# Kernel optimization log

Measured on AMD Instinct MI355X. Metric: run time of the kernel, lower is better.

Reference implementation:

```python
import jax, jax.numpy as jnp
import numpy as np

B, T, C = 2, 1024, 1024
E, F, K = 8, 2048, 2


def setup_inputs() -> dict:
    key = jax.random.key(0)
    ks = jax.random.split(key, 5)
    s = 1.0 / np.sqrt(C)
    return {
        "x": jax.random.normal(ks[0], (B, T, C), jnp.float32),
        "Wr": jax.random.normal(ks[1], (E, C), jnp.float32) * s,   # router weight [E, d_model]
        "w1": jax.random.normal(ks[2], (E, C, F), jnp.float32) * s, # gate proj per expert
        "w3": jax.random.normal(ks[3], (E, C, F), jnp.float32) * s, # up proj per expert
        "w2": jax.random.normal(ks[4], (E, F, C), jnp.float32) * (1.0 / np.sqrt(F)),  # down proj
    }


def reference(x, Wr, w1, w3, w2):
    Bq, Tq, Cq = x.shape
    flat = x.reshape(-1, Cq)                          # [N, C]
    N = flat.shape[0]
    probs = jax.nn.softmax(flat @ Wr.T, axis=-1)      # [N, E]
    topw, topi = jax.lax.top_k(probs, K)              # [N, K]
    topw = topw / jnp.sum(topw, axis=-1, keepdims=True)
    # dense gate matrix: zero for unselected experts (same math as masked loop)
    gates = jnp.zeros((N, E), flat.dtype).at[jnp.arange(N)[:, None], topi].set(topw)
    # evaluate all experts, weight by gates (gate=0 kills unrouted experts)
    h1 = jnp.einsum('nd,edf->nef', flat, w1)          # [N, E, F]
    h3 = jnp.einsum('nd,edf->nef', flat, w3)
    h = jax.nn.silu(h1) * h3
    y = jnp.einsum('nef,efd->ned', h, w2)             # [N, E, C]
    out = jnp.einsum('ned,ne->nd', y, gates)          # [N, C]
    return out.reshape(Bq, Tq, Cq)
```

## Files before the change

kernel.cpp:

```cpp
#include <hip/hip_runtime.h>
#include <math.h>

typedef _Float16 f16;
typedef _Float16 f16x2 __attribute__((ext_vector_type(2)));
typedef _Float16 f16x4 __attribute__((ext_vector_type(4)));
typedef _Float16 f16x8 __attribute__((ext_vector_type(8)));
typedef __fp16 h16x2 __attribute__((ext_vector_type(2)));
typedef float f32x4 __attribute__((ext_vector_type(4)));
typedef float f32x16 __attribute__((ext_vector_type(16)));

#define N_TOK 2048
#define C_DIM 1024
#define E_NUM 8
#define F_DIM 2048
#define BM 256

#define WS_COUNTS    0
#define WS_OFFSETS   64
#define WS_CURSOR    192
#define WS_TOPI      256
#define WS_TOPW      (WS_TOPI + 16384)
#define WS_ROWS      (WS_TOPW + 16384)
#define WS_SLOT      (WS_ROWS + 16384)
#define WS_X16       (1u << 20)
#define WS_H         (6u << 20)
#define WS_Y0        (23u << 20)
#define WS_Y1        (32u << 20)

__device__ __forceinline__ void glds16(const void* g, void* l) {
  __builtin_amdgcn_global_load_lds((const __attribute__((address_space(1))) void*)g,
                                   (__attribute__((address_space(3))) void*)l, 16, 0, 0);
}

__device__ __forceinline__ f16x2 pkrtz(float a, float b) {
  union { h16x2 h; f16x2 f; } u;
  u.h = __builtin_amdgcn_cvt_pkrtz(a, b);
  return u.f;
}

__global__ void cvtx_kernel(const float* __restrict__ x, f16* __restrict__ x16) {
  int i = (blockIdx.x * 256 + threadIdx.x) * 8;
  f32x4 a = *(const f32x4*)(x + i);
  f32x4 b = *(const f32x4*)(x + i + 4);
  union { f16x8 v; f16x2 h[4]; } u;
  u.h[0] = pkrtz(a[0], a[1]);
  u.h[1] = pkrtz(a[2], a[3]);
  u.h[2] = pkrtz(b[0], b[1]);
  u.h[3] = pkrtz(b[2], b[3]);
  *(f16x8*)(x16 + i) = u.v;
}

__global__ void router_kernel(const float* __restrict__ x, const float* __restrict__ Wr,
                              int* counts, int* topi, float* topw) {
  int tok = blockIdx.x * 4 + (threadIdx.x >> 6);
  int lane = threadIdx.x & 63;
  const float* xr = x + (size_t)tok * C_DIM;
  float xv[16];
#pragma unroll
  for (int i = 0; i < 16; ++i) xv[i] = xr[i * 64 + lane];
  float logit[E_NUM];
#pragma unroll
  for (int e = 0; e < E_NUM; ++e) {
    const float* wr = Wr + (size_t)e * C_DIM;
    float acc = 0.f;
#pragma unroll
    for (int i = 0; i < 16; ++i) acc += xv[i] * wr[i * 64 + lane];
#pragma unroll
    for (int s = 1; s < 64; s <<= 1) acc += __shfl_xor(acc, s, 64);
    logit[e] = acc;
  }
  if (lane == 0) {
    float m = logit[0];
#pragma unroll
    for (int e = 1; e < E_NUM; ++e) m = fmaxf(m, logit[e]);
    float p[E_NUM];
#pragma unroll
    for (int e = 0; e < E_NUM; ++e) p[e] = expf(logit[e] - m);
    float p0 = -1.f, p1 = -1.f;
    int i0 = 0, i1 = 0;
#pragma unroll
    for (int e = 0; e < E_NUM; ++e) {
      float v = p[e];
      if (v > p0) { p1 = p0; i1 = i0; p0 = v; i0 = e; }
      else if (v > p1) { p1 = v; i1 = e; }
    }
    float inv = 1.f / (p0 + p1);
    topi[2 * tok] = i0; topi[2 * tok + 1] = i1;
    topw[2 * tok] = p0 * inv; topw[2 * tok + 1] = p1 * inv;
    atomicAdd(&counts[i0], 1);
    atomicAdd(&counts[i1], 1);
  }
}

__global__ void scan_kernel(const int* counts, int* offsets, int* cursor) {
  if (threadIdx.x == 0) {
    int o = 0;
    for (int e = 0; e < E_NUM; ++e) {
      offsets[e] = o; cursor[e] = o;
      o += counts[e];
    }
    offsets[E_NUM] = o;
  }
}

__global__ void scatter_kernel(const int* __restrict__ topi, int* cursor,
                               int* rows_perm, int* slot_of) {
  int n = blockIdx.x * blockDim.x + threadIdx.x;
  if (n >= N_TOK) return;
#pragma unroll
  for (int k = 0; k < 2; ++k) {
    int e = topi[2 * n + k];
    int pos = atomicAdd(&cursor[e], 1);
    rows_perm[pos] = n;
    slot_of[2 * n + k] = pos;
  }
}

#define UP_STEP(R1, R3)                                                          \
  do {                                                                           \
    { union { f16x8 v; f16x2 h[4]; } u;                                          \
      u.h[0] = pkrtz(R1[0], R1[1]); u.h[1] = pkrtz(R1[2], R1[3]);                \
      u.h[2] = pkrtz(R1[4], R1[5]); u.h[3] = pkrtz(R1[6], R1[7]);                \
      *(f16x8*)&B1_lds[cur][bso] = u.v;                                          \
      u.h[0] = pkrtz(R3[0], R3[1]); u.h[1] = pkrtz(R3[2], R3[3]);                \
      u.h[2] = pkrtz(R3[4], R3[5]); u.h[3] = pkrtz(R3[6], R3[7]);                \
      *(f16x8*)&B3_lds[cur][bso] = u.v; }                                        \
    asm volatile("s_waitcnt lgkmcnt(0)" ::: "memory");                           \
    __builtin_amdgcn_s_barrier();                                                \
    { int kn = ((ti + 2) & 31) * 32;                                             \
      _Pragma("unroll") for (int j = 0; j < 8; ++j) {                            \
        R1[j] = w1p[(size_t)(kn + j) * F_DIM];                                   \
        R3[j] = w3p[(size_t)(kn + j) * F_DIM]; }                                 \
      glds16(asrc[0] + kn, a_wr + wid * 512);                                    \
      glds16(asrc[1] + kn, a_wr + (8 + wid) * 512); }                            \
    asm volatile("s_waitcnt vmcnt(36)" ::: "memory");                            \
    { f16x8 a[2][2], b[2][2];                                                    \
      _Pragma("unroll") for (int mi = 0; mi < 2; ++mi)                           \
        _Pragma("unroll") for (int kk = 0; kk < 2; ++kk) {                       \
          int row = wr + mi * 32 + ln31;                                         \
          int cell = kk * 2 + fh;                                                \
          a[mi][kk] = *(const f16x8*)&a_rd0[row * 32 + (cell ^ ((row >> 1) & 3)) * 8]; } \
      _Pragma("unroll") for (int ni = 0; ni < 2; ++ni)                           \
        _Pragma("unroll") for (int kk = 0; kk < 2; ++kk) {                       \
          int col = wc + ni * 32 + ln31;                                         \
          int cell = kk * 2 + fh;                                                \
          b[ni][kk] = *(const f16x8*)&B1_lds[cur][col * 32 + (cell ^ ((col >> 1) & 3)) * 8]; } \
      _Pragma("unroll") for (int kk = 0; kk < 2; ++kk)                           \
        _Pragma("unroll") for (int mi = 0; mi < 2; ++mi)                         \
          _Pragma("unroll") for (int ni = 0; ni < 2; ++ni)                       \
            acc1[mi][ni] = __builtin_amdgcn_mfma_f32_32x32x16_f16(a[mi][kk], b[ni][kk], acc1[mi][ni], 0, 0, 0); \
      _Pragma("unroll") for (int ni = 0; ni < 2; ++ni)                           \
        _Pragma("unroll") for (int kk = 0; kk < 2; ++kk) {                       \
          int col = wc + ni * 32 + ln31;                                         \
          int cell = kk * 2 + fh;                                                \
          b[ni][kk] = *(const f16x8*)&B3_lds[cur][col * 32 + (cell ^ ((col >> 1) & 3)) * 8]; } \
      _Pragma("unroll") for (int kk = 0; kk < 2; ++kk)                           \
        _Pragma("unroll") for (int mi = 0; mi < 2; ++mi)                         \
          _Pragma("unroll") for (int ni = 0; ni < 2; ++ni)                       \
            acc3[mi][ni] = __builtin_amdgcn_mfma_f32_32x32x16_f16(a[mi][kk], b[ni][kk], acc3[mi][ni], 0, 0, 0); } \
    { f16* _t = a_rd0; a_rd0 = a_rd1; a_rd1 = a_wr; a_wr = _t; }                 \
    ++ti; cur ^= 1;                                                              \
  } while (0)

__launch_bounds__(512, 2)
__global__ void upproj_kernel(const f16* __restrict__ x16,
                              const float* __restrict__ w1,
                              const float* __restrict__ w3,
                              const int* __restrict__ counts,
                              const int* __restrict__ offsets,
                              const int* __restrict__ rows_perm,
                              f16* __restrict__ h_buf) {
  __shared__ f16 A_lds[3][BM * 32];
  __shared__ f16 B1_lds[2][128 * 32];
  __shared__ f16 B3_lds[2][128 * 32];

  int bid = blockIdx.x;
  int e = bid & 7;
  int slot = bid >> 3;
  int tile = slot & 7;
  int fidx = slot >> 3;
  int cnt = counts[e];
  if (tile * BM >= cnt) return;
  int row0 = tile * BM;
  int off = offsets[e];
  int f0 = fidx * 128;
  int t = threadIdx.x, wid = t >> 6, lane = t & 63;
  int ln31 = lane & 31, fh = lane >> 5;

  const f16* asrc[2];
#pragma unroll
  for (int p = 0; p < 2; ++p) {
    int c = (p * 8 + wid) * 64 + lane;
    int row = c >> 2, cc = c & 3;
    int lr = row0 + row; if (lr > cnt - 1) lr = cnt - 1;
    int g = rows_perm[off + lr];
    asrc[p] = x16 + (size_t)g * C_DIM + 8 * (cc ^ ((row >> 1) & 3));
  }

  int bcol = t & 127, kg = t >> 7;
  int bso = bcol * 32 + (kg ^ ((bcol >> 1) & 3)) * 8;
  const size_t eb = (size_t)e * C_DIM * F_DIM;
  const float* w1p = w1 + eb + (size_t)(kg * 8) * F_DIM + f0 + bcol;
  const float* w3p = w3 + eb + (size_t)(kg * 8) * F_DIM + f0 + bcol;

  f32x16 acc1[2][2] = {};
  f32x16 acc3[2][2] = {};
  int wr = (wid >> 1) * 64, wc = (wid & 1) * 64;

  f16* a_rd0 = &A_lds[0][0];
  f16* a_rd1 = &A_lds[1][0];
  f16* a_wr  = &A_lds[2][0];

  float rA1[8], rA3[8], rB1[8], rB3[8];
#pragma unroll
  for (int j = 0; j < 8; ++j) { rA1[j] = w1p[(size_t)j * F_DIM]; rA3[j] = w3p[(size_t)j * F_DIM]; }
  glds16(asrc[0], a_rd0 + wid * 512);
  glds16(asrc[1], a_rd0 + (8 + wid) * 512);
#pragma unroll
  for (int j = 0; j < 8; ++j) { rB1[j] = w1p[(size_t)(32 + j) * F_DIM]; rB3[j] = w3p[(size_t)(32 + j) * F_DIM]; }
  glds16(asrc[0] + 32, a_rd1 + wid * 512);
  glds16(asrc[1] + 32, a_rd1 + (8 + wid) * 512);

  int ti = 0, cur = 0;
  for (int tp = 0; tp < 16; ++tp) {
    UP_STEP(rA1, rA3);
    UP_STEP(rB1, rB3);
  }

#pragma unroll
  for (int mi = 0; mi < 2; ++mi)
#pragma unroll
    for (int ni = 0; ni < 2; ++ni)
#pragma unroll
      for (int i = 0; i < 16; ++i) {
        int rr = (i & 3) + 8 * (i >> 2) + 4 * fh;
        int lr = row0 + wr + mi * 32 + rr;
        if (lr < cnt) {
          float v1 = acc1[mi][ni][i], v3 = acc3[mi][ni][i];
          float hval = v1 / (1.f + expf(-v1)) * v3;
          h_buf[(size_t)(off + lr) * F_DIM + f0 + wc + ni * 32 + ln31] = (f16)hval;
        }
      }
}

#define DN_STEP(RB)                                                              \
  do {                                                                           \
    { union { f16x8 v; f16x2 h[4]; } u;                                          \
      u.h[0] = pkrtz(RB[0], RB[1]); u.h[1] = pkrtz(RB[2], RB[3]);                \
      u.h[2] = pkrtz(RB[4], RB[5]); u.h[3] = pkrtz(RB[6], RB[7]);                \
      *(f16x8*)&B_lds[cur][bso] = u.v; }                                         \
    asm volatile("s_waitcnt lgkmcnt(0)" ::: "memory");                           \
    __builtin_amdgcn_s_barrier();                                                \
    { int kn = ((ti + 2) & 31) * 32;                                             \
      _Pragma("unroll") for (int j = 0; j < 8; ++j)                              \
        RB[j] = w2p[(size_t)(kn + j) * C_DIM];                                   \
      glds16(asrc[0] + kn, a_wr + wid * 512);                                    \
      glds16(asrc[1] + kn, a_wr + (8 + wid) * 512); }                            \
    asm volatile("s_waitcnt vmcnt(20)" ::: "memory");                            \
    { f16x8 a[2][2], b[2][2];                                                    \
      _Pragma("unroll") for (int mi = 0; mi < 2; ++mi)                           \
        _Pragma("unroll") for (int kk = 0; kk < 2; ++kk) {                       \
          int row = wr + mi * 32 + ln31;                                         \
          int cell = kk * 2 + fh;                                                \
          a[mi][kk] = *(const f16x8*)&a_rd0[row * 32 + (cell ^ ((row >> 1) & 3)) * 8]; } \
      _Pragma("unroll") for (int ni = 0; ni < 2; ++ni)                           \
        _Pragma("unroll") for (int kk = 0; kk < 2; ++kk) {                       \
          int col = wc + ni * 32 + ln31;                                         \
          int cell = kk * 2 + fh;                                                \
          b[ni][kk] = *(const f16x8*)&B_lds[cur][col * 32 + (cell ^ ((col >> 1) & 3)) * 8]; } \
      _Pragma("unroll") for (int kk = 0; kk < 2; ++kk)                           \
        _Pragma("unroll") for (int mi = 0; mi < 2; ++mi)                         \
          _Pragma("unroll") for (int ni = 0; ni < 2; ++ni)                       \
            acc[mi][ni] = __builtin_amdgcn_mfma_f32_32x32x16_f16(a[mi][kk], b[ni][kk], acc[mi][ni], 0, 0, 0); } \
    { f16* _t = a_rd0; a_rd0 = a_rd1; a_rd1 = a_wr; a_wr = _t; }                 \
    ++ti; cur ^= 1;                                                              \
  } while (0)

__launch_bounds__(512, 2)
__global__ void downproj_kernel(const f16* __restrict__ h_buf,
                                const float* __restrict__ w2,
                                const int* __restrict__ counts,
                                const int* __restrict__ offsets,
                                f16* __restrict__ y0,
                                f16* __restrict__ y1) {
  __shared__ f16 A_lds[3][BM * 32];
  __shared__ f16 B_lds[2][128 * 32];

  int bid = blockIdx.x;
  int e = bid & 7;
  int slot = bid >> 3;
  int tile = slot & 7;
  int kh = (slot >> 3) & 1;
  int cidx = slot >> 4;
  int cnt = counts[e];
  if (tile * BM >= cnt) return;
  f16* yb = kh ? y1 : y0;
  int row0 = tile * BM;
  int off = offsets[e];
  int c0 = cidx * 128;
  int t = threadIdx.x, wid = t >> 6, lane = t & 63;
  int ln31 = lane & 31, fh = lane >> 5;

  const f16* asrc[2];
#pragma unroll
  for (int p = 0; p < 2; ++p) {
    int c = (p * 8 + wid) * 64 + lane;
    int row = c >> 2, cc = c & 3;
    int lr = row0 + row; if (lr > cnt - 1) lr = cnt - 1;
    asrc[p] = h_buf + (size_t)(off + lr) * F_DIM + kh * 1024 + 8 * (cc ^ ((row >> 1) & 3));
  }

  int bcol = t & 127, kg = t >> 7;
  int bso = bcol * 32 + (kg ^ ((bcol >> 1) & 3)) * 8;
  const float* w2p = w2 + (size_t)e * F_DIM * C_DIM
                     + (size_t)(kh * 1024 + kg * 8) * C_DIM + c0 + bcol;

  f32x16 acc[2][2] = {};
  int wr = (wid >> 1) * 64, wc = (wid & 1) * 64;

  f16* a_rd0 = &A_lds[0][0];
  f16* a_rd1 = &A_lds[1][0];
  f16* a_wr  = &A_lds[2][0];

  float rA[8], rB[8];
#pragma unroll
  for (int j = 0; j < 8; ++j) rA[j] = w2p[(size_t)j * C_DIM];
  glds16(asrc[0], a_rd0 + wid * 512);
  glds16(asrc[1], a_rd0 + (8 + wid) * 512);
#pragma unroll
  for (int j = 0; j < 8; ++j) rB[j] = w2p[(size_t)(32 + j) * C_DIM];
  glds16(asrc[0] + 32, a_rd1 + wid * 512);
  glds16(asrc[1] + 32, a_rd1 + (8 + wid) * 512);

  int ti = 0, cur = 0;
  for (int tp = 0; tp < 16; ++tp) {
    DN_STEP(rA);
    DN_STEP(rB);
  }

#pragma unroll
  for (int mi = 0; mi < 2; ++mi)
#pragma unroll
    for (int ni = 0; ni < 2; ++ni)
#pragma unroll
      for (int i = 0; i < 16; ++i) {
        int rr = (i & 3) + 8 * (i >> 2) + 4 * fh;
        int lr = row0 + wr + mi * 32 + rr;
        if (lr < cnt)
          yb[(size_t)(off + lr) * C_DIM + c0 + wc + ni * 32 + ln31] = (f16)acc[mi][ni][i];
      }
}

__global__ void combine_kernel(const f16* __restrict__ y0, const f16* __restrict__ y1,
                               const int* __restrict__ slot_of,
                               const float* __restrict__ topw,
                               float* __restrict__ out) {
  int n = blockIdx.x;
  int s0 = slot_of[2 * n], s1 = slot_of[2 * n + 1];
  float g0 = topw[2 * n], g1 = topw[2 * n + 1];
  int c = threadIdx.x * 4;
  f16x4 a0 = *(const f16x4*)(y0 + (size_t)s0 * C_DIM + c);
  f16x4 a1 = *(const f16x4*)(y1 + (size_t)s0 * C_DIM + c);
  f16x4 b0 = *(const f16x4*)(y0 + (size_t)s1 * C_DIM + c);
  f16x4 b1 = *(const f16x4*)(y1 + (size_t)s1 * C_DIM + c);
  f32x4 o;
#pragma unroll
  for (int i = 0; i < 4; ++i)
    o[i] = g0 * ((float)a0[i] + (float)a1[i]) + g1 * ((float)b0[i] + (float)b1[i]);
  *(f32x4*)(out + (size_t)n * C_DIM + c) = o;
}

extern "C" void kernel_launch(void* const* d_in, const int* in_sizes, int n_in,
                              void* d_out, int out_size, void* d_ws, size_t ws_size,
                              hipStream_t stream) {
  const float* x  = (const float*)d_in[0];
  const float* Wr = (const float*)d_in[1];
  const float* w1 = (const float*)d_in[2];
  const float* w3 = (const float*)d_in[3];
  const float* w2 = (const float*)d_in[4];
  float* out = (float*)d_out;
  char* ws = (char*)d_ws;

  int* counts    = (int*)(ws + WS_COUNTS);
  int* offsets   = (int*)(ws + WS_OFFSETS);
  int* cursor    = (int*)(ws + WS_CURSOR);
  int* topi      = (int*)(ws + WS_TOPI);
  float* topw    = (float*)(ws + WS_TOPW);
  int* rows_perm = (int*)(ws + WS_ROWS);
  int* slot_of   = (int*)(ws + WS_SLOT);
  f16* x16       = (f16*)(ws + WS_X16);
  f16* h_buf     = (f16*)(ws + WS_H);
  f16* y0        = (f16*)(ws + WS_Y0);
  f16* y1        = (f16*)(ws + WS_Y1);

  (void)hipMemsetAsync(ws, 0, 256, stream);
  cvtx_kernel<<<N_TOK * C_DIM / 8 / 256, 256, 0, stream>>>(x, x16);
  router_kernel<<<N_TOK / 4, 256, 0, stream>>>(x, Wr, counts, topi, topw);
  scan_kernel<<<1, 64, 0, stream>>>(counts, offsets, cursor);
  scatter_kernel<<<N_TOK / 256, 256, 0, stream>>>(topi, cursor, rows_perm, slot_of);
  upproj_kernel<<<E_NUM * 128, 512, 0, stream>>>(
      x16, w1, w3, counts, offsets, rows_perm, h_buf);
  downproj_kernel<<<E_NUM * 128, 512, 0, stream>>>(
      h_buf, w2, counts, offsets, y0, y1);
  combine_kernel<<<N_TOK, 256, 0, stream>>>(y0, y1, slot_of, topw, out);
}
```

Before: 240.1 us.

## Pre-transpose weights to fp16 and stream all GEMM operands directly into LDS

Adds a per-call kernel that converts w1, w3 and w2 to fp16 and transposes them to a K-contiguous layout. The up- and down-projection GEMMs can then load the weight tiles with direct global-to-LDS loads into a triple-buffered pipeline, instead of loading fp32 into registers, converting, and storing to LDS. It also reorders block indexing so that neighbouring blocks share weight columns, and raises MFMA issue priority. The cost is an extra full read and write pass over all expert weights on every call.

```diff
diff --git a/kernel.cpp b/kernel.cpp
--- a/kernel.cpp
+++ b/kernel.cpp
@@ -22,10 +22,13 @@
 #define WS_TOPW      (WS_TOPI + 16384)
 #define WS_ROWS      (WS_TOPW + 16384)
 #define WS_SLOT      (WS_ROWS + 16384)
-#define WS_X16       (1u << 20)
-#define WS_H         (6u << 20)
-#define WS_Y0        (23u << 20)
-#define WS_Y1        (32u << 20)
+#define WS_X16       (1ull << 20)
+#define WS_H         (6ull << 20)
+#define WS_Y0        (23ull << 20)
+#define WS_Y1        (32ull << 20)
+#define WS_W1T       (48ull << 20)
+#define WS_W3T       (80ull << 20)
+#define WS_W2T       (112ull << 20)
 
 __device__ __forceinline__ void glds16(const void* g, void* l) {
   __builtin_amdgcn_global_load_lds((const __attribute__((address_space(1))) void*)g,
@@ -50,6 +53,41 @@
   *(f16x8*)(x16 + i) = u.v;
 }
 
+__global__ void wt_kernel(const float* __restrict__ w1, const float* __restrict__ w3,
+                          const float* __restrict__ w2,
+                          f16* __restrict__ w1t, f16* __restrict__ w3t, f16* __restrict__ w2t) {
+  __shared__ __align__(16) f16 T[128 * 132];
+  int tid = blockIdx.x;
+  int m = tid >> 10;
+  int r = tid & 1023;
+  int e = r >> 7;
+  int tl = r & 127;
+  const float* src; f16* dst; int K, Fd, kt, ft;
+  if (m == 2) { K = F_DIM; Fd = C_DIM; kt = tl >> 3; ft = tl & 7; src = w2; dst = w2t; }
+  else        { K = C_DIM; Fd = F_DIM; kt = tl >> 4; ft = tl & 15; src = (m ? w3 : w1); dst = (m ? w3t : w1t); }
+  src += ((size_t)e * K + kt * 128) * Fd + ft * 128;
+  dst += ((size_t)e * Fd + ft * 128) * K + kt * 128;
+  int t = threadIdx.x;
+  int rr = t >> 5, c4 = (t & 31) * 4;
+#pragma unroll
+  for (int it = 0; it < 16; ++it) {
+    int k = it * 8 + rr;
+    f32x4 v = *(const f32x4*)(src + (size_t)k * Fd + c4);
+    union { f16x4 q; f16x2 h[2]; } u;
+    u.h[0] = pkrtz(v[0], v[1]); u.h[1] = pkrtz(v[2], v[3]);
+    *(f16x4*)&T[k * 132 + c4] = u.q;
+  }
+  __syncthreads();
+  int f = t >> 1, kh = t & 1;
+#pragma unroll
+  for (int j8 = 0; j8 < 8; ++j8) {
+    union { f16x8 v; f16 s[8]; } u;
+#pragma unroll
+    for (int jj = 0; jj < 8; ++jj) u.s[jj] = T[(kh * 64 + j8 * 8 + jj) * 132 + f];
+    *(f16x8*)(dst + (size_t)f * K + kh * 64 + j8 * 8) = u.v;
+  }
+}
+
 __global__ void router_kernel(const float* __restrict__ x, const float* __restrict__ Wr,
                               int* counts, int* topi, float* topw) {
   int tok = blockIdx.x * 4 + (threadIdx.x >> 6);
@@ -116,69 +154,57 @@
   }
 }
 
-#define UP_STEP(R1, R3)                                                          \
+#define ROT3(P0, P1, P2) { f16* _t = P0; P0 = P1; P1 = P2; P2 = _t; }
+
+#define UP_MFMA()                                                                \
   do {                                                                           \
-    { union { f16x8 v; f16x2 h[4]; } u;                                          \
-      u.h[0] = pkrtz(R1[0], R1[1]); u.h[1] = pkrtz(R1[2], R1[3]);                \
-      u.h[2] = pkrtz(R1[4], R1[5]); u.h[3] = pkrtz(R1[6], R1[7]);                \
-      *(f16x8*)&B1_lds[cur][bso] = u.v;                                          \
-      u.h[0] = pkrtz(R3[0], R3[1]); u.h[1] = pkrtz(R3[2], R3[3]);                \
-      u.h[2] = pkrtz(R3[4], R3[5]); u.h[3] = pkrtz(R3[6], R3[7]);                \
-      *(f16x8*)&B3_lds[cur][bso] = u.v; }                                        \
-    asm volatile("s_waitcnt lgkmcnt(0)" ::: "memory");                           \
-    __builtin_amdgcn_s_barrier();                                                \
-    { int kn = ((ti + 2) & 31) * 32;                                             \
-      _Pragma("unroll") for (int j = 0; j < 8; ++j) {                            \
-        R1[j] = w1p[(size_t)(kn + j) * F_DIM];                                   \
-        R3[j] = w3p[(size_t)(kn + j) * F_DIM]; }                                 \
-      glds16(asrc[0] + kn, a_wr + wid * 512);                                    \
-      glds16(asrc[1] + kn, a_wr + (8 + wid) * 512); }                            \
-    asm volatile("s_waitcnt vmcnt(36)" ::: "memory");                            \
-    { f16x8 a[2][2], b[2][2];                                                    \
+    f16x8 a[2][2], b[2][2];                                                      \
+    _Pragma("unroll") for (int mi = 0; mi < 2; ++mi)                             \
+      _Pragma("unroll") for (int kk = 0; kk < 2; ++kk) {                         \
+        int row = wr + mi * 32 + ln31;                                           \
+        int cell = kk * 2 + fh;                                                  \
+        a[mi][kk] = *(const f16x8*)&a_c[row * 32 + (cell ^ ((row >> 1) & 3)) * 8]; } \
+    _Pragma("unroll") for (int ni = 0; ni < 2; ++ni)                             \
+      _Pragma("unroll") for (int kk = 0; kk < 2; ++kk) {                         \
+        int col = wc + ni * 32 + ln31;                                           \
+        int cell = kk * 2 + fh;                                                  \
+        b[ni][kk] = *(const f16x8*)&b1_c[col * 32 + (cell ^ ((col >> 1) & 3)) * 8]; } \
+    __builtin_amdgcn_s_setprio(1);                                               \
+    _Pragma("unroll") for (int kk = 0; kk < 2; ++kk)                             \
       _Pragma("unroll") for (int mi = 0; mi < 2; ++mi)                           \
-        _Pragma("unroll") for (int kk = 0; kk < 2; ++kk) {                       \
-          int row = wr + mi * 32 + ln31;                                         \
-          int cell = kk * 2 + fh;                                                \
-          a[mi][kk] = *(const f16x8*)&a_rd0[row * 32 + (cell ^ ((row >> 1) & 3)) * 8]; } \
-      _Pragma("unroll") for (int ni = 0; ni < 2; ++ni)                           \
-        _Pragma("unroll") for (int kk = 0; kk < 2; ++kk) {                       \
-          int col = wc + ni * 32 + ln31;                                         \
-          int cell = kk * 2 + fh;                                                \
-          b[ni][kk] = *(const f16x8*)&B1_lds[cur][col * 32 + (cell ^ ((col >> 1) & 3)) * 8]; } \
-      _Pragma("unroll") for (int kk = 0; kk < 2; ++kk)                           \
-        _Pragma("unroll") for (int mi = 0; mi < 2; ++mi)                         \
-          _Pragma("unroll") for (int ni = 0; ni < 2; ++ni)                       \
-            acc1[mi][ni] = __builtin_amdgcn_mfma_f32_32x32x16_f16(a[mi][kk], b[ni][kk], acc1[mi][ni], 0, 0, 0); \
-      _Pragma("unroll") for (int ni = 0; ni < 2; ++ni)                           \
-        _Pragma("unroll") for (int kk = 0; kk < 2; ++kk) {                       \
-          int col = wc + ni * 32 + ln31;                                         \
-          int cell = kk * 2 + fh;                                                \
-          b[ni][kk] = *(const f16x8*)&B3_lds[cur][col * 32 + (cell ^ ((col >> 1) & 3)) * 8]; } \
-      _Pragma("unroll") for (int kk = 0; kk < 2; ++kk)                           \
-        _Pragma("unroll") for (int mi = 0; mi < 2; ++mi)                         \
-          _Pragma("unroll") for (int ni = 0; ni < 2; ++ni)                       \
-            acc3[mi][ni] = __builtin_amdgcn_mfma_f32_32x32x16_f16(a[mi][kk], b[ni][kk], acc3[mi][ni], 0, 0, 0); } \
-    { f16* _t = a_rd0; a_rd0 = a_rd1; a_rd1 = a_wr; a_wr = _t; }                 \
-    ++ti; cur ^= 1;                                                              \
+        _Pragma("unroll") for (int ni = 0; ni < 2; ++ni)                         \
+          acc1[mi][ni] = __builtin_amdgcn_mfma_f32_32x32x16_f16(a[mi][kk], b[ni][kk], acc1[mi][ni], 0, 0, 0); \
+    __builtin_amdgcn_s_setprio(0);                                               \
+    _Pragma("unroll") for (int ni = 0; ni < 2; ++ni)                             \
+      _Pragma("unroll") for (int kk = 0; kk < 2; ++kk) {                         \
+        int col = wc + ni * 32 + ln31;                                           \
+        int cell = kk * 2 + fh;                                                  \
+        b[ni][kk] = *(const f16x8*)&b3_c[col * 32 + (cell ^ ((col >> 1) & 3)) * 8]; } \
+    __builtin_amdgcn_s_setprio(1);                                               \
+    _Pragma("unroll") for (int kk = 0; kk < 2; ++kk)                             \
+      _Pragma("unroll") for (int mi = 0; mi < 2; ++mi)                           \
+        _Pragma("unroll") for (int ni = 0; ni < 2; ++ni)                         \
+          acc3[mi][ni] = __builtin_amdgcn_mfma_f32_32x32x16_f16(a[mi][kk], b[ni][kk], acc3[mi][ni], 0, 0, 0); \
+    __builtin_amdgcn_s_setprio(0);                                               \
   } while (0)
 
 __launch_bounds__(512, 2)
 __global__ void upproj_kernel(const f16* __restrict__ x16,
-                              const float* __restrict__ w1,
-                              const float* __restrict__ w3,
+                              const f16* __restrict__ w1t,
+                              const f16* __restrict__ w3t,
                               const int* __restrict__ counts,
                               const int* __restrict__ offsets,
                               const int* __restrict__ rows_perm,
                               f16* __restrict__ h_buf) {
-  __shared__ f16 A_lds[3][BM * 32];
-  __shared__ f16 B1_lds[2][128 * 32];
-  __shared__ f16 B3_lds[2][128 * 32];
+  __shared__ __align__(16) f16 A_lds[3][BM * 32];
+  __shared__ __align__(16) f16 B1_lds[3][128 * 32];
+  __shared__ __align__(16) f16 B3_lds[3][128 * 32];
 
   int bid = blockIdx.x;
   int e = bid & 7;
   int slot = bid >> 3;
-  int tile = slot & 7;
-  int fidx = slot >> 3;
+  int fidx = slot & 15;
+  int tile = slot >> 4;
   int cnt = counts[e];
   if (tile * BM >= cnt) return;
   int row0 = tile * BM;
@@ -190,42 +216,55 @@
   const f16* asrc[2];
 #pragma unroll
   for (int p = 0; p < 2; ++p) {
-    int c = (p * 8 + wid) * 64 + lane;
+    int c = p * 512 + t;
     int row = c >> 2, cc = c & 3;
     int lr = row0 + row; if (lr > cnt - 1) lr = cnt - 1;
     int g = rows_perm[off + lr];
     asrc[p] = x16 + (size_t)g * C_DIM + 8 * (cc ^ ((row >> 1) & 3));
   }
-
-  int bcol = t & 127, kg = t >> 7;
-  int bso = bcol * 32 + (kg ^ ((bcol >> 1) & 3)) * 8;
-  const size_t eb = (size_t)e * C_DIM * F_DIM;
-  const float* w1p = w1 + eb + (size_t)(kg * 8) * F_DIM + f0 + bcol;
-  const float* w3p = w3 + eb + (size_t)(kg * 8) * F_DIM + f0 + bcol;
+  int bcol = t >> 2, bcc = t & 3;
+  int bswz = 8 * (bcc ^ ((bcol >> 1) & 3));
+  const f16* b1src = w1t + (size_t)e * F_DIM * C_DIM + (size_t)(f0 + bcol) * C_DIM + bswz;
+  const f16* b3src = w3t + (size_t)e * F_DIM * C_DIM + (size_t)(f0 + bcol) * C_DIM + bswz;
 
   f32x16 acc1[2][2] = {};
   f32x16 acc3[2][2] = {};
   int wr = (wid >> 1) * 64, wc = (wid & 1) * 64;
 
-  f16* a_rd0 = &A_lds[0][0];
-  f16* a_rd1 = &A_lds[1][0];
-  f16* a_wr  = &A_lds[2][0];
-
-  float rA1[8], rA3[8], rB1[8], rB3[8];
-#pragma unroll
-  for (int j = 0; j < 8; ++j) { rA1[j] = w1p[(size_t)j * F_DIM]; rA3[j] = w3p[(size_t)j * F_DIM]; }
-  glds16(asrc[0], a_rd0 + wid * 512);
-  glds16(asrc[1], a_rd0 + (8 + wid) * 512);
-#pragma unroll
-  for (int j = 0; j < 8; ++j) { rB1[j] = w1p[(size_t)(32 + j) * F_DIM]; rB3[j] = w3p[(size_t)(32 + j) * F_DIM]; }
-  glds16(asrc[0] + 32, a_rd1 + wid * 512);
-  glds16(asrc[1] + 32, a_rd1 + (8 + wid) * 512);
-
-  int ti = 0, cur = 0;
-  for (int tp = 0; tp < 16; ++tp) {
-    UP_STEP(rA1, rA3);
-    UP_STEP(rB1, rB3);
-  }
+  f16 *a_c = &A_lds[0][0], *a_n = &A_lds[1][0], *a_f = &A_lds[2][0];
+  f16 *b1_c = &B1_lds[0][0], *b1_n = &B1_lds[1][0], *b1_f = &B1_lds[2][0];
+  f16 *b3_c = &B3_lds[0][0], *b3_n = &B3_lds[1][0], *b3_f = &B3_lds[2][0];
+
+  glds16(asrc[0], a_c + wid * 512);
+  glds16(asrc[1], a_c + (8 + wid) * 512);
+  glds16(b1src, b1_c + wid * 512);
+  glds16(b3src, b3_c + wid * 512);
+  glds16(asrc[0] + 32, a_n + wid * 512);
+  glds16(asrc[1] + 32, a_n + (8 + wid) * 512);
+  glds16(b1src + 32, b1_n + wid * 512);
+  glds16(b3src + 32, b3_n + wid * 512);
+
+  for (int tt = 0; tt < 30; ++tt) {
+    asm volatile("s_waitcnt vmcnt(4)" ::: "memory");
+    __builtin_amdgcn_s_barrier();
+    asm volatile("" ::: "memory");
+    int kn = (tt + 2) * 32;
+    glds16(asrc[0] + kn, a_f + wid * 512);
+    glds16(asrc[1] + kn, a_f + (8 + wid) * 512);
+    glds16(b1src + kn, b1_f + wid * 512);
+    glds16(b3src + kn, b3_f + wid * 512);
+    UP_MFMA();
+    ROT3(a_c, a_n, a_f); ROT3(b1_c, b1_n, b1_f); ROT3(b3_c, b3_n, b3_f);
+  }
+  asm volatile("s_waitcnt vmcnt(4)" ::: "memory");
+  __builtin_amdgcn_s_barrier();
+  asm volatile("" ::: "memory");
+  UP_MFMA();
+  ROT3(a_c, a_n, a_f); ROT3(b1_c, b1_n, b1_f); ROT3(b3_c, b3_n, b3_f);
+  asm volatile("s_waitcnt vmcnt(0)" ::: "memory");
+  __builtin_amdgcn_s_barrier();
+  asm volatile("" ::: "memory");
+  UP_MFMA();
 
 #pragma unroll
   for (int mi = 0; mi < 2; ++mi)
@@ -243,55 +282,43 @@
       }
 }
 
-#define DN_STEP(RB)                                                              \
+#define DN_MFMA()                                                                \
   do {                                                                           \
-    { union { f16x8 v; f16x2 h[4]; } u;                                          \
-      u.h[0] = pkrtz(RB[0], RB[1]); u.h[1] = pkrtz(RB[2], RB[3]);                \
-      u.h[2] = pkrtz(RB[4], RB[5]); u.h[3] = pkrtz(RB[6], RB[7]);                \
-      *(f16x8*)&B_lds[cur][bso] = u.v; }                                         \
-    asm volatile("s_waitcnt lgkmcnt(0)" ::: "memory");                           \
-    __builtin_amdgcn_s_barrier();                                                \
-    { int kn = ((ti + 2) & 31) * 32;                                             \
-      _Pragma("unroll") for (int j = 0; j < 8; ++j)                              \
-        RB[j] = w2p[(size_t)(kn + j) * C_DIM];                                   \
-      glds16(asrc[0] + kn, a_wr + wid * 512);                                    \
-      glds16(asrc[1] + kn, a_wr + (8 + wid) * 512); }                            \
-    asm volatile("s_waitcnt vmcnt(20)" ::: "memory");                            \
-    { f16x8 a[2][2], b[2][2];                                                    \
+    f16x8 a[2][2], b[2][2];                                                      \
+    _Pragma("unroll") for (int mi = 0; mi < 2; ++mi)                             \
+      _Pragma("unroll") for (int kk = 0; kk < 2; ++kk) {                         \
+        int row = wr + mi * 32 + ln31;                                           \
+        int cell = kk * 2 + fh;                                                  \
+        a[mi][kk] = *(const f16x8*)&a_c[row * 32 + (cell ^ ((row >> 1) & 3)) * 8]; } \
+    _Pragma("unroll") for (int ni = 0; ni < 2; ++ni)                             \
+      _Pragma("unroll") for (int kk = 0; kk < 2; ++kk) {                         \
+        int col = wc + ni * 32 + ln31;                                           \
+        int cell = kk * 2 + fh;                                                  \
+        b[ni][kk] = *(const f16x8*)&b_c[col * 32 + (cell ^ ((col >> 1) & 3)) * 8]; } \
+    __builtin_amdgcn_s_setprio(1);                                               \
+    _Pragma("unroll") for (int kk = 0; kk < 2; ++kk)                             \
       _Pragma("unroll") for (int mi = 0; mi < 2; ++mi)                           \
-        _Pragma("unroll") for (int kk = 0; kk < 2; ++kk) {                       \
-          int row = wr + mi * 32 + ln31;                                         \
-          int cell = kk * 2 + fh;                                                \
-          a[mi][kk] = *(const f16x8*)&a_rd0[row * 32 + (cell ^ ((row >> 1) & 3)) * 8]; } \
-      _Pragma("unroll") for (int ni = 0; ni < 2; ++ni)                           \
-        _Pragma("unroll") for (int kk = 0; kk < 2; ++kk) {                       \
-          int col = wc + ni * 32 + ln31;                                         \
-          int cell = kk * 2 + fh;                                                \
-          b[ni][kk] = *(const f16x8*)&B_lds[cur][col * 32 + (cell ^ ((col >> 1) & 3)) * 8]; } \
-      _Pragma("unroll") for (int kk = 0; kk < 2; ++kk)                           \
-        _Pragma("unroll") for (int mi = 0; mi < 2; ++mi)                         \
-          _Pragma("unroll") for (int ni = 0; ni < 2; ++ni)                       \
-            acc[mi][ni] = __builtin_amdgcn_mfma_f32_32x32x16_f16(a[mi][kk], b[ni][kk], acc[mi][ni], 0, 0, 0); } \
-    { f16* _t = a_rd0; a_rd0 = a_rd1; a_rd1 = a_wr; a_wr = _t; }                 \
-    ++ti; cur ^= 1;                                                              \
+        _Pragma("unroll") for (int ni = 0; ni < 2; ++ni)                         \
+          acc[mi][ni] = __builtin_amdgcn_mfma_f32_32x32x16_f16(a[mi][kk], b[ni][kk], acc[mi][ni], 0, 0, 0); \
+    __builtin_amdgcn_s_setprio(0);                                               \
   } while (0)
 
 __launch_bounds__(512, 2)
 __global__ void downproj_kernel(const f16* __restrict__ h_buf,
-                                const float* __restrict__ w2,
+                                const f16* __restrict__ w2t,
                                 const int* __restrict__ counts,
                                 const int* __restrict__ offsets,
                                 f16* __restrict__ y0,
                                 f16* __restrict__ y1) {
-  __shared__ f16 A_lds[3][BM * 32];
-  __shared__ f16 B_lds[2][128 * 32];
+  __shared__ __align__(16) f16 A_lds[3][BM * 32];
+  __shared__ __align__(16) f16 B_lds[3][128 * 32];
 
   int bid = blockIdx.x;
   int e = bid & 7;
   int slot = bid >> 3;
-  int tile = slot & 7;
+  int cidx = slot & 7;
   int kh = (slot >> 3) & 1;
-  int cidx = slot >> 4;
+  int tile = slot >> 4;
   int cnt = counts[e];
   if (tile * BM >= cnt) return;
   f16* yb = kh ? y1 : y0;
@@ -304,39 +331,48 @@
   const f16* asrc[2];
 #pragma unroll
   for (int p = 0; p < 2; ++p) {
-    int c = (p * 8 + wid) * 64 + lane;
+    int c = p * 512 + t;
     int row = c >> 2, cc = c & 3;
     int lr = row0 + row; if (lr > cnt - 1) lr = cnt - 1;
     asrc[p] = h_buf + (size_t)(off + lr) * F_DIM + kh * 1024 + 8 * (cc ^ ((row >> 1) & 3));
   }
-
-  int bcol = t & 127, kg = t >> 7;
-  int bso = bcol * 32 + (kg ^ ((bcol >> 1) & 3)) * 8;
-  const float* w2p = w2 + (size_t)e * F_DIM * C_DIM
-                     + (size_t)(kh * 1024 + kg * 8) * C_DIM + c0 + bcol;
+  int bcol = t >> 2, bcc = t & 3;
+  const f16* bsrc = w2t + (size_t)e * C_DIM * F_DIM + (size_t)(c0 + bcol) * F_DIM
+                    + kh * 1024 + 8 * (bcc ^ ((bcol >> 1) & 3));
 
   f32x16 acc[2][2] = {};
   int wr = (wid >> 1) * 64, wc = (wid & 1) * 64;
 
-  f16* a_rd0 = &A_lds[0][0];
-  f16* a_rd1 = &A_lds[1][0];
-  f16* a_wr  = &A_lds[2][0];
-
-  float rA[8], rB[8];
-#pragma unroll
-  for (int j = 0; j < 8; ++j) rA[j] = w2p[(size_t)j * C_DIM];
-  glds16(asrc[0], a_rd0 + wid * 512);
-  glds16(asrc[1], a_rd0 + (8 + wid) * 512);
-#pragma unroll
-  for (int j = 0; j < 8; ++j) rB[j] = w2p[(size_t)(32 + j) * C_DIM];
-  glds16(asrc[0] + 32, a_rd1 + wid * 512);
-  glds16(asrc[1] + 32, a_rd1 + (8 + wid) * 512);
-
-  int ti = 0, cur = 0;
-  for (int tp = 0; tp < 16; ++tp) {
-    DN_STEP(rA);
-    DN_STEP(rB);
-  }
+  f16 *a_c = &A_lds[0][0], *a_n = &A_lds[1][0], *a_f = &A_lds[2][0];
+  f16 *b_c = &B_lds[0][0], *b_n = &B_lds[1][0], *b_f = &B_lds[2][0];
+
+  glds16(asrc[0], a_c + wid * 512);
+  glds16(asrc[1], a_c + (8 + wid) * 512);
+  glds16(bsrc, b_c + wid * 512);
+  glds16(asrc[0] + 32, a_n + wid * 512);
+  glds16(asrc[1] + 32, a_n + (8 + wid) * 512);
+  glds16(bsrc + 32, b_n + wid * 512);
+
+  for (int tt = 0; tt < 30; ++tt) {
+    asm volatile("s_waitcnt vmcnt(3)" ::: "memory");
+    __builtin_amdgcn_s_barrier();
+    asm volatile("" ::: "memory");
+    int kn = (tt + 2) * 32;
+    glds16(asrc[0] + kn, a_f + wid * 512);
+    glds16(asrc[1] + kn, a_f + (8 + wid) * 512);
+    glds16(bsrc + kn, b_f + wid * 512);
+    DN_MFMA();
+    ROT3(a_c, a_n, a_f); ROT3(b_c, b_n, b_f);
+  }
+  asm volatile("s_waitcnt vmcnt(3)" ::: "memory");
+  __builtin_amdgcn_s_barrier();
+  asm volatile("" ::: "memory");
+  DN_MFMA();
+  ROT3(a_c, a_n, a_f); ROT3(b_c, b_n, b_f);
+  asm volatile("s_waitcnt vmcnt(0)" ::: "memory");
+  __builtin_amdgcn_s_barrier();
+  asm volatile("" ::: "memory");
+  DN_MFMA();
 
 #pragma unroll
   for (int mi = 0; mi < 2; ++mi)
@@ -392,15 +428,19 @@
   f16* h_buf     = (f16*)(ws + WS_H);
   f16* y0        = (f16*)(ws + WS_Y0);
   f16* y1        = (f16*)(ws + WS_Y1);
+  f16* w1t       = (f16*)(ws + WS_W1T);
+  f16* w3t       = (f16*)(ws + WS_W3T);
+  f16* w2t       = (f16*)(ws + WS_W2T);
 
   (void)hipMemsetAsync(ws, 0, 256, stream);
+  wt_kernel<<<3072, 256, 0, stream>>>(w1, w3, w2, w1t, w3t, w2t);
   cvtx_kernel<<<N_TOK * C_DIM / 8 / 256, 256, 0, stream>>>(x, x16);
   router_kernel<<<N_TOK / 4, 256, 0, stream>>>(x, Wr, counts, topi, topw);
   scan_kernel<<<1, 64, 0, stream>>>(counts, offsets, cursor);
   scatter_kernel<<<N_TOK / 256, 256, 0, stream>>>(topi, cursor, rows_perm, slot_of);
   upproj_kernel<<<E_NUM * 128, 512, 0, stream>>>(
-      x16, w1, w3, counts, offsets, rows_perm, h_buf);
+      x16, w1t, w3t, counts, offsets, rows_perm, h_buf);
   downproj_kernel<<<E_NUM * 128, 512, 0, stream>>>(
-      h_buf, w2, counts, offsets, y0, y1);
+      h_buf, w2t, counts, offsets, y0, y1);
   combine_kernel<<<N_TOK, 256, 0, stream>>>(y0, y1, slot_of, topw, out);
 }
```

New measurement: 261.7 us. 1.09x slower.

## Load A operands directly to registers, drop LDS A staging, reorder grid

Applied to the files above, without the earlier changes.

Both expert GEMM kernels stop staging activation tiles through LDS with global_load_lds triple buffering. Each wave now loads its A fragments straight from global memory into registers, double-buffered between steps. The B weight prefetch is cut from two register sets to one, and s_setprio is wrapped around the MFMA blocks. Block index decoding is reordered so neighbouring blocks share the same row tile, which should improve L2 reuse of activations. The risks are more global loads per wave (four waves read the same A rows), shallower latency hiding for the weights, and removal of the explicit vmcnt waits.

```diff
diff --git a/kernel.cpp b/kernel.cpp
--- a/kernel.cpp
+++ b/kernel.cpp
@@ -22,15 +22,10 @@
 #define WS_TOPW      (WS_TOPI + 16384)
 #define WS_ROWS      (WS_TOPW + 16384)
 #define WS_SLOT      (WS_ROWS + 16384)
-#define WS_X16       (1u << 20)
-#define WS_H         (6u << 20)
-#define WS_Y0        (23u << 20)
-#define WS_Y1        (32u << 20)
-
-__device__ __forceinline__ void glds16(const void* g, void* l) {
-  __builtin_amdgcn_global_load_lds((const __attribute__((address_space(1))) void*)g,
-                                   (__attribute__((address_space(3))) void*)l, 16, 0, 0);
-}
+#define WS_X16       (1ull << 20)
+#define WS_H         (6ull << 20)
+#define WS_Y0        (23ull << 20)
+#define WS_Y1        (32ull << 20)
 
 __device__ __forceinline__ f16x2 pkrtz(float a, float b) {
   union { h16x2 h; f16x2 f; } u;
@@ -116,51 +111,56 @@
   }
 }
 
-#define UP_STEP(R1, R3)                                                          \
-  do {                                                                           \
-    { union { f16x8 v; f16x2 h[4]; } u;                                          \
-      u.h[0] = pkrtz(R1[0], R1[1]); u.h[1] = pkrtz(R1[2], R1[3]);                \
-      u.h[2] = pkrtz(R1[4], R1[5]); u.h[3] = pkrtz(R1[6], R1[7]);                \
-      *(f16x8*)&B1_lds[cur][bso] = u.v;                                          \
-      u.h[0] = pkrtz(R3[0], R3[1]); u.h[1] = pkrtz(R3[2], R3[3]);                \
-      u.h[2] = pkrtz(R3[4], R3[5]); u.h[3] = pkrtz(R3[6], R3[7]);                \
-      *(f16x8*)&B3_lds[cur][bso] = u.v; }                                        \
-    asm volatile("s_waitcnt lgkmcnt(0)" ::: "memory");                           \
-    __builtin_amdgcn_s_barrier();                                                \
-    { int kn = ((ti + 2) & 31) * 32;                                             \
-      _Pragma("unroll") for (int j = 0; j < 8; ++j) {                            \
-        R1[j] = w1p[(size_t)(kn + j) * F_DIM];                                   \
-        R3[j] = w3p[(size_t)(kn + j) * F_DIM]; }                                 \
-      glds16(asrc[0] + kn, a_wr + wid * 512);                                    \
-      glds16(asrc[1] + kn, a_wr + (8 + wid) * 512); }                            \
-    asm volatile("s_waitcnt vmcnt(36)" ::: "memory");                            \
-    { f16x8 a[2][2], b[2][2];                                                    \
-      _Pragma("unroll") for (int mi = 0; mi < 2; ++mi)                           \
-        _Pragma("unroll") for (int kk = 0; kk < 2; ++kk) {                       \
-          int row = wr + mi * 32 + ln31;                                         \
-          int cell = kk * 2 + fh;                                                \
-          a[mi][kk] = *(const f16x8*)&a_rd0[row * 32 + (cell ^ ((row >> 1) & 3)) * 8]; } \
-      _Pragma("unroll") for (int ni = 0; ni < 2; ++ni)                           \
-        _Pragma("unroll") for (int kk = 0; kk < 2; ++kk) {                       \
-          int col = wc + ni * 32 + ln31;                                         \
-          int cell = kk * 2 + fh;                                                \
-          b[ni][kk] = *(const f16x8*)&B1_lds[cur][col * 32 + (cell ^ ((col >> 1) & 3)) * 8]; } \
-      _Pragma("unroll") for (int kk = 0; kk < 2; ++kk)                           \
-        _Pragma("unroll") for (int mi = 0; mi < 2; ++mi)                         \
-          _Pragma("unroll") for (int ni = 0; ni < 2; ++ni)                       \
-            acc1[mi][ni] = __builtin_amdgcn_mfma_f32_32x32x16_f16(a[mi][kk], b[ni][kk], acc1[mi][ni], 0, 0, 0); \
-      _Pragma("unroll") for (int ni = 0; ni < 2; ++ni)                           \
-        _Pragma("unroll") for (int kk = 0; kk < 2; ++kk) {                       \
-          int col = wc + ni * 32 + ln31;                                         \
-          int cell = kk * 2 + fh;                                                \
-          b[ni][kk] = *(const f16x8*)&B3_lds[cur][col * 32 + (cell ^ ((col >> 1) & 3)) * 8]; } \
-      _Pragma("unroll") for (int kk = 0; kk < 2; ++kk)                           \
-        _Pragma("unroll") for (int mi = 0; mi < 2; ++mi)                         \
-          _Pragma("unroll") for (int ni = 0; ni < 2; ++ni)                       \
-            acc3[mi][ni] = __builtin_amdgcn_mfma_f32_32x32x16_f16(a[mi][kk], b[ni][kk], acc3[mi][ni], 0, 0, 0); } \
-    { f16* _t = a_rd0; a_rd0 = a_rd1; a_rd1 = a_wr; a_wr = _t; }                 \
-    ++ti; cur ^= 1;                                                              \
-  } while (0)
+#define BARRIER_PUB()                                          \
+  asm volatile("s_waitcnt lgkmcnt(0)" ::: "memory");           \
+  __builtin_amdgcn_s_barrier();                                \
+  asm volatile("" ::: "memory");
+
+#define UP_PACK_WRITE()                                                  \
+  { union { f16x8 v; f16x2 h[4]; } u;                                    \
+    u.h[0] = pkrtz(b1r[0], b1r[1]); u.h[1] = pkrtz(b1r[2], b1r[3]);      \
+    u.h[2] = pkrtz(b1r[4], b1r[5]); u.h[3] = pkrtz(b1r[6], b1r[7]);      \
+    *(f16x8*)&B1_lds[cur][bso] = u.v;                                    \
+    u.h[0] = pkrtz(b3r[0], b3r[1]); u.h[1] = pkrtz(b3r[2], b3r[3]);      \
+    u.h[2] = pkrtz(b3r[4], b3r[5]); u.h[3] = pkrtz(b3r[6], b3r[7]);      \
+    *(f16x8*)&B3_lds[cur][bso] = u.v; }
+
+#define UP_LOAD(ANXT, KN)                                                \
+  { _Pragma("unroll") for (int j = 0; j < 8; ++j) {                      \
+      b1r[j] = w1p[(size_t)(KN + j) * F_DIM];                            \
+      b3r[j] = w3p[(size_t)(KN + j) * F_DIM]; }                          \
+    _Pragma("unroll") for (int mi = 0; mi < 2; ++mi)                     \
+      _Pragma("unroll") for (int kk = 0; kk < 2; ++kk)                   \
+        ANXT[mi][kk] = *(const f16x8*)(aptr[mi] + (KN) + kk * 16 + fh * 8); }
+
+#define UP_MFMA(ACUR)                                                    \
+  { f16x8 bf[2][2];                                                      \
+    _Pragma("unroll") for (int ni = 0; ni < 2; ++ni)                     \
+      _Pragma("unroll") for (int kk = 0; kk < 2; ++kk) {                 \
+        int col = wc + ni * 32 + ln31;                                   \
+        int cell = (kk * 2 + fh) ^ ((col >> 1) & 3);                     \
+        bf[ni][kk] = *(const f16x8*)&B1_lds[cur][col * 32 + cell * 8]; } \
+    __builtin_amdgcn_s_setprio(1);                                       \
+    _Pragma("unroll") for (int kk = 0; kk < 2; ++kk)                     \
+      _Pragma("unroll") for (int mi = 0; mi < 2; ++mi)                   \
+        _Pragma("unroll") for (int ni = 0; ni < 2; ++ni)                 \
+          acc1[mi][ni] = __builtin_amdgcn_mfma_f32_32x32x16_f16(ACUR[mi][kk], bf[ni][kk], acc1[mi][ni], 0, 0, 0); \
+    __builtin_amdgcn_s_setprio(0);                                       \
+    _Pragma("unroll") for (int ni = 0; ni < 2; ++ni)                     \
+      _Pragma("unroll") for (int kk = 0; kk < 2; ++kk) {                 \
+        int col = wc + ni * 32 + ln31;                                   \
+        int cell = (kk * 2 + fh) ^ ((col >> 1) & 3);                     \
+        bf[ni][kk] = *(const f16x8*)&B3_lds[cur][col * 32 + cell * 8]; } \
+    __builtin_amdgcn_s_setprio(1);                                       \
+    _Pragma("unroll") for (int kk = 0; kk < 2; ++kk)                     \
+      _Pragma("unroll") for (int mi = 0; mi < 2; ++mi)                   \
+        _Pragma("unroll") for (int ni = 0; ni < 2; ++ni)                 \
+          acc3[mi][ni] = __builtin_amdgcn_mfma_f32_32x32x16_f16(ACUR[mi][kk], bf[ni][kk], acc3[mi][ni], 0, 0, 0); \
+    __builtin_amdgcn_s_setprio(0);                                       \
+    cur ^= 1; }
+
+#define UP_STEP(ACUR, ANXT, KN) \
+  { UP_PACK_WRITE(); UP_LOAD(ANXT, KN); BARRIER_PUB(); UP_MFMA(ACUR); }
 
 __launch_bounds__(512, 2)
 __global__ void upproj_kernel(const f16* __restrict__ x16,
@@ -170,15 +170,14 @@
                               const int* __restrict__ offsets,
                               const int* __restrict__ rows_perm,
                               f16* __restrict__ h_buf) {
-  __shared__ f16 A_lds[3][BM * 32];
-  __shared__ f16 B1_lds[2][128 * 32];
-  __shared__ f16 B3_lds[2][128 * 32];
+  __shared__ __align__(16) f16 B1_lds[2][128 * 32];
+  __shared__ __align__(16) f16 B3_lds[2][128 * 32];
 
   int bid = blockIdx.x;
   int e = bid & 7;
   int slot = bid >> 3;
-  int tile = slot & 7;
-  int fidx = slot >> 3;
+  int fidx = slot & 15;
+  int tile = slot >> 4;
   int cnt = counts[e];
   if (tile * BM >= cnt) return;
   int row0 = tile * BM;
@@ -186,46 +185,35 @@
   int f0 = fidx * 128;
   int t = threadIdx.x, wid = t >> 6, lane = t & 63;
   int ln31 = lane & 31, fh = lane >> 5;
-
-  const f16* asrc[2];
-#pragma unroll
-  for (int p = 0; p < 2; ++p) {
-    int c = (p * 8 + wid) * 64 + lane;
-    int row = c >> 2, cc = c & 3;
-    int lr = row0 + row; if (lr > cnt - 1) lr = cnt - 1;
-    int g = rows_perm[off + lr];
-    asrc[p] = x16 + (size_t)g * C_DIM + 8 * (cc ^ ((row >> 1) & 3));
+  int wr = (wid >> 1) * 64, wc = (wid & 1) * 64;
+
+  const f16* aptr[2];
+#pragma unroll
+  for (int mi = 0; mi < 2; ++mi) {
+    int lr = row0 + wr + mi * 32 + ln31;
+    if (lr > cnt - 1) lr = cnt - 1;
+    aptr[mi] = x16 + (size_t)rows_perm[off + lr] * C_DIM;
   }
 
   int bcol = t & 127, kg = t >> 7;
-  int bso = bcol * 32 + (kg ^ ((bcol >> 1) & 3)) * 8;
+  int bso = bcol * 32 + ((kg ^ ((bcol >> 1) & 3)) * 8);
   const size_t eb = (size_t)e * C_DIM * F_DIM;
   const float* w1p = w1 + eb + (size_t)(kg * 8) * F_DIM + f0 + bcol;
   const float* w3p = w3 + eb + (size_t)(kg * 8) * F_DIM + f0 + bcol;
 
   f32x16 acc1[2][2] = {};
   f32x16 acc3[2][2] = {};
-  int wr = (wid >> 1) * 64, wc = (wid & 1) * 64;
-
-  f16* a_rd0 = &A_lds[0][0];
-  f16* a_rd1 = &A_lds[1][0];
-  f16* a_wr  = &A_lds[2][0];
-
-  float rA1[8], rA3[8], rB1[8], rB3[8];
-#pragma unroll
-  for (int j = 0; j < 8; ++j) { rA1[j] = w1p[(size_t)j * F_DIM]; rA3[j] = w3p[(size_t)j * F_DIM]; }
-  glds16(asrc[0], a_rd0 + wid * 512);
-  glds16(asrc[1], a_rd0 + (8 + wid) * 512);
-#pragma unroll
-  for (int j = 0; j < 8; ++j) { rB1[j] = w1p[(size_t)(32 + j) * F_DIM]; rB3[j] = w3p[(size_t)(32 + j) * F_DIM]; }
-  glds16(asrc[0] + 32, a_rd1 + wid * 512);
-  glds16(asrc[1] + 32, a_rd1 + (8 + wid) * 512);
-
-  int ti = 0, cur = 0;
-  for (int tp = 0; tp < 16; ++tp) {
-    UP_STEP(rA1, rA3);
-    UP_STEP(rB1, rB3);
-  }
+  float b1r[8], b3r[8];
+  f16x8 aX[2][2], aY[2][2];
+  int cur = 0;
+
+  UP_LOAD(aX, 0);
+  for (int tp = 0; tp < 15; ++tp) {
+    UP_STEP(aX, aY, (2 * tp + 1) * 32);
+    UP_STEP(aY, aX, (2 * tp + 2) * 32);
+  }
+  UP_STEP(aX, aY, 31 * 32);
+  { UP_PACK_WRITE(); BARRIER_PUB(); UP_MFMA(aY); }
 
 #pragma unroll
   for (int mi = 0; mi < 2; ++mi)
@@ -243,38 +231,36 @@
       }
 }
 
-#define DN_STEP(RB)                                                              \
-  do {                                                                           \
-    { union { f16x8 v; f16x2 h[4]; } u;                                          \
-      u.h[0] = pkrtz(RB[0], RB[1]); u.h[1] = pkrtz(RB[2], RB[3]);                \
-      u.h[2] = pkrtz(RB[4], RB[5]); u.h[3] = pkrtz(RB[6], RB[7]);                \
-      *(f16x8*)&B_lds[cur][bso] = u.v; }                                         \
-    asm volatile("s_waitcnt lgkmcnt(0)" ::: "memory");                           \
-    __builtin_amdgcn_s_barrier();                                                \
-    { int kn = ((ti + 2) & 31) * 32;                                             \
-      _Pragma("unroll") for (int j = 0; j < 8; ++j)                              \
-        RB[j] = w2p[(size_t)(kn + j) * C_DIM];                                   \
-      glds16(asrc[0] + kn, a_wr + wid * 512);                                    \
-      glds16(asrc[1] + kn, a_wr + (8 + wid) * 512); }                            \
-    asm volatile("s_waitcnt vmcnt(20)" ::: "memory");                            \
-    { f16x8 a[2][2], b[2][2];                                                    \
-      _Pragma("unroll") for (int mi = 0; mi < 2; ++mi)                           \
-        _Pragma("unroll") for (int kk = 0; kk < 2; ++kk) {                       \
-          int row = wr + mi * 32 + ln31;                                         \
-          int cell = kk * 2 + fh;                                                \
-          a[mi][kk] = *(const f16x8*)&a_rd0[row * 32 + (cell ^ ((row >> 1) & 3)) * 8]; } \
-      _Pragma("unroll") for (int ni = 0; ni < 2; ++ni)                           \
-        _Pragma("unroll") for (int kk = 0; kk < 2; ++kk) {                       \
-          int col = wc + ni * 32 + ln31;                                         \
-          int cell = kk * 2 + fh;                                                \
-          b[ni][kk] = *(const f16x8*)&B_lds[cur][col * 32 + (cell ^ ((col >> 1) & 3)) * 8]; } \
-      _Pragma("unroll") for (int kk = 0; kk < 2; ++kk)                           \
-        _Pragma("unroll") for (int mi = 0; mi < 2; ++mi)                         \
-          _Pragma("unroll") for (int ni = 0; ni < 2; ++ni)                       \
-            acc[mi][ni] = __builtin_amdgcn_mfma_f32_32x32x16_f16(a[mi][kk], b[ni][kk], acc[mi][ni], 0, 0, 0); } \
-    { f16* _t = a_rd0; a_rd0 = a_rd1; a_rd1 = a_wr; a_wr = _t; }                 \
-    ++ti; cur ^= 1;                                                              \
-  } while (0)
+#define DN_PACK_WRITE()                                                  \
+  { union { f16x8 v; f16x2 h[4]; } u;                                    \
+    u.h[0] = pkrtz(br[0], br[1]); u.h[1] = pkrtz(br[2], br[3]);          \
+    u.h[2] = pkrtz(br[4], br[5]); u.h[3] = pkrtz(br[6], br[7]);          \
+    *(f16x8*)&B_lds[cur][bso] = u.v; }
+
+#define DN_LOAD(ANXT, KN)                                                \
+  { _Pragma("unroll") for (int j = 0; j < 8; ++j)                        \
+      br[j] = w2p[(size_t)(KN + j) * C_DIM];                             \
+    _Pragma("unroll") for (int mi = 0; mi < 2; ++mi)                     \
+      _Pragma("unroll") for (int kk = 0; kk < 2; ++kk)                   \
+        ANXT[mi][kk] = *(const f16x8*)(aptr[mi] + (KN) + kk * 16 + fh * 8); }
+
+#define DN_MFMA(ACUR)                                                    \
+  { f16x8 bf[2][2];                                                      \
+    _Pragma("unroll") for (int ni = 0; ni < 2; ++ni)                     \
+      _Pragma("unroll") for (int kk = 0; kk < 2; ++kk) {                 \
+        int col = wc + ni * 32 + ln31;                                   \
+        int cell = (kk * 2 + fh) ^ ((col >> 1) & 3);                     \
+        bf[ni][kk] = *(const f16x8*)&B_lds[cur][col * 32 + cell * 8]; }  \
+    __builtin_amdgcn_s_setprio(1);                                       \
+    _Pragma("unroll") for (int kk = 0; kk < 2; ++kk)                     \
+      _Pragma("unroll") for (int mi = 0; mi < 2; ++mi)                   \
+        _Pragma("unroll") for (int ni = 0; ni < 2; ++ni)                 \
+          acc[mi][ni] = __builtin_amdgcn_mfma_f32_32x32x16_f16(ACUR[mi][kk], bf[ni][kk], acc[mi][ni], 0, 0, 0); \
+    __builtin_amdgcn_s_setprio(0);                                       \
+    cur ^= 1; }
+
+#define DN_STEP(ACUR, ANXT, KN) \
+  { DN_PACK_WRITE(); DN_LOAD(ANXT, KN); BARRIER_PUB(); DN_MFMA(ACUR); }
 
 __launch_bounds__(512, 2)
 __global__ void downproj_kernel(const f16* __restrict__ h_buf,
@@ -283,15 +269,14 @@
                                 const int* __restrict__ offsets,
                                 f16* __restrict__ y0,
                                 f16* __restrict__ y1) {
-  __shared__ f16 A_lds[3][BM * 32];
-  __shared__ f16 B_lds[2][128 * 32];
+  __shared__ __align__(16) f16 B_lds[2][128 * 32];
 
   int bid = blockIdx.x;
   int e = bid & 7;
   int slot = bid >> 3;
-  int tile = slot & 7;
+  int cidx = slot & 7;
   int kh = (slot >> 3) & 1;
-  int cidx = slot >> 4;
+  int tile = slot >> 4;
   int cnt = counts[e];
   if (tile * BM >= cnt) return;
   f16* yb = kh ? y1 : y0;
@@ -300,43 +285,33 @@
   int c0 = cidx * 128;
   int t = threadIdx.x, wid = t >> 6, lane = t & 63;
   int ln31 = lane & 31, fh = lane >> 5;
-
-  const f16* asrc[2];
-#pragma unroll
-  for (int p = 0; p < 2; ++p) {
-    int c = (p * 8 + wid) * 64 + lane;
-    int row = c >> 2, cc = c & 3;
-    int lr = row0 + row; if (lr > cnt - 1) lr = cnt - 1;
-    asrc[p] = h_buf + (size_t)(off + lr) * F_DIM + kh * 1024 + 8 * (cc ^ ((row >> 1) & 3));
+  int wr = (wid >> 1) * 64, wc = (wid & 1) * 64;
+
+  const f16* aptr[2];
+#pragma unroll
+  for (int mi = 0; mi < 2; ++mi) {
+    int lr = row0 + wr + mi * 32 + ln31;
+    if (lr > cnt - 1) lr = cnt - 1;
+    aptr[mi] = h_buf + (size_t)(off + lr) * F_DIM + kh * 1024;
   }
 
   int bcol = t & 127, kg = t >> 7;
-  int bso = bcol * 32 + (kg ^ ((bcol >> 1) & 3)) * 8;
+  int bso = bcol * 32 + ((kg ^ ((bcol >> 1) & 3)) * 8);
   const float* w2p = w2 + (size_t)e * F_DIM * C_DIM
                      + (size_t)(kh * 1024 + kg * 8) * C_DIM + c0 + bcol;
 
   f32x16 acc[2][2] = {};
-  int wr = (wid >> 1) * 64, wc = (wid & 1) * 64;
-
-  f16* a_rd0 = &A_lds[0][0];
-  f16* a_rd1 = &A_lds[1][0];
-  f16* a_wr  = &A_lds[2][0];
-
-  float rA[8], rB[8];
-#pragma unroll
-  for (int j = 0; j < 8; ++j) rA[j] = w2p[(size_t)j * C_DIM];
-  glds16(asrc[0], a_rd0 + wid * 512);
-  glds16(asrc[1], a_rd0 + (8 + wid) * 512);
-#pragma unroll
-  for (int j = 0; j < 8; ++j) rB[j] = w2p[(size_t)(32 + j) * C_DIM];
-  glds16(asrc[0] + 32, a_rd1 + wid * 512);
-  glds16(asrc[1] + 32, a_rd1 + (8 + wid) * 512);
-
-  int ti = 0, cur = 0;
-  for (int tp = 0; tp < 16; ++tp) {
-    DN_STEP(rA);
-    DN_STEP(rB);
-  }
+  float br[8];
+  f16x8 aX[2][2], aY[2][2];
+  int cur = 0;
+
+  DN_LOAD(aX, 0);
+  for (int tp = 0; tp < 15; ++tp) {
+    DN_STEP(aX, aY, (2 * tp + 1) * 32);
+    DN_STEP(aY, aX, (2 * tp + 2) * 32);
+  }
+  DN_STEP(aX, aY, 31 * 32);
+  { DN_PACK_WRITE(); BARRIER_PUB(); DN_MFMA(aY); }
 
 #pragma unroll
   for (int mi = 0; mi < 2; ++mi)
```

Measured after the change: 234.7 us. 1.02x faster.
